# Optimization experiments

Measured on AMD Instinct MI355X. Metric: run time of the kernel, lower is better.

The kernel has to match this reference:

```python
import jax, jax.numpy as jnp
import numpy as np

N = 100000   # nodes
E = 500000   # edges
DN = 64      # node feat dim
DE = 64      # edge feat dim
D = 128      # hidden = in_feats = out_feats
TD = 64      # time-encoding dim


def setup_inputs() -> dict:
    key = jax.random.key(0)
    ks = jax.random.split(key, 20)
    s = 0.05
    inp = {
        'nfeat': jax.random.normal(ks[0], (N, DN), dtype=jnp.float32),
        'efeat': jax.random.normal(ks[1], (E, DE), dtype=jnp.float32),
        'src': jax.random.randint(ks[2], (E,), 0, N),
        'dst': jax.random.randint(ks[3], (E,), 0, N),
        'ts': jax.random.uniform(ks[4], (E,), dtype=jnp.float32) * 1000.0,
    }
    i = 5
    for l in (1, 2):
        inp[f'W_self{l}'] = jax.random.normal(ks[i], (D + TD, D), dtype=jnp.float32) * s; i += 1
        inp[f'b_self{l}'] = jnp.zeros((D,), dtype=jnp.float32)
        inp[f'W_neigh{l}'] = jax.random.normal(ks[i], (D, D), dtype=jnp.float32) * s; i += 1
        inp[f'b_neigh{l}'] = jnp.zeros((D,), dtype=jnp.float32)
        inp[f'omega{l}'] = jax.random.normal(ks[i], (TD,), dtype=jnp.float32); i += 1
        inp[f'phase{l}'] = jax.random.normal(ks[i], (TD,), dtype=jnp.float32); i += 1
    return inp


def _tsage_layer(src_prev, dst_prev, src, dst, ts, W_self, b_self, W_neigh, b_neigh, omega, phase):
    # cosine time encoding per edge: [E, TD]
    te = jnp.cos(ts[:, None] * omega[None, :] + phase[None, :])
    # temporal-neighborhood mean: per node, mean of features of incident edges
    sum_n = (jax.ops.segment_sum(dst_prev, src, num_segments=N)
             + jax.ops.segment_sum(src_prev, dst, num_segments=N))      # [N, D]
    ones = jnp.ones((src.shape[0], 1), dtype=src_prev.dtype)
    cnt = (jax.ops.segment_sum(ones, src, num_segments=N)
           + jax.ops.segment_sum(ones, dst, num_segments=N))            # [N, 1]
    mean_n = sum_n / jnp.maximum(cnt, 1.0)                              # [N, D]
    neigh_proj = mean_n @ W_neigh + b_neigh                             # project once per node
    src_out = jnp.concatenate([src_prev, te], axis=1) @ W_self + b_self + neigh_proj[src]
    dst_out = jnp.concatenate([dst_prev, te], axis=1) @ W_self + b_self + neigh_proj[dst]
    # dropout in eval mode (identity), then activation (relu)
    return jax.nn.relu(src_out), jax.nn.relu(dst_out)


def reference(nfeat, efeat, src, dst, ts,
              W_self1, b_self1, W_neigh1, b_neigh1, omega1, phase1,
              W_self2, b_self2, W_neigh2, b_neigh2, omega2, phase2):
    # combine_feats: per-edge gather-concat of endpoint node feats with edge feats
    src_feat = jnp.concatenate([nfeat[src], efeat], axis=1)  # [E, D]
    dst_feat = jnp.concatenate([nfeat[dst], efeat], axis=1)  # [E, D]
    params = [
        (W_self1, b_self1, W_neigh1, b_neigh1, omega1, phase1),
        (W_self2, b_self2, W_neigh2, b_neigh2, omega2, phase2),
    ]
    for p in params:
        src_feat, dst_feat = _tsage_layer(src_feat, dst_feat, src, dst, ts, *p)
    return src_feat, dst_feat
```

## Files before the change

### kernel.cpp

```cpp
#include <hip/hip_runtime.h>
#include <cstdint>
#include <cmath>

#define NN 100000
#define EE 500000
#define CAP 48

typedef __attribute__((ext_vector_type(8))) short short8v;
typedef __attribute__((ext_vector_type(4))) float f32x4;

static __device__ __forceinline__ unsigned short f2bf_rne(float x) {
    unsigned u = __float_as_uint(x);
    u += 0x7FFFu + ((u >> 16) & 1u);
    return (unsigned short)(u >> 16);
}

static __device__ __forceinline__ void split8(float4 a, float4 b,
                                              short8v* hi, short8v* lo) {
    union { short8v v; unsigned u[4]; } H, L;
    float f[8] = {a.x, a.y, a.z, a.w, b.x, b.y, b.z, b.w};
#pragma unroll
    for (int p = 0; p < 4; ++p) {
        unsigned u0 = __float_as_uint(f[2 * p]);
        unsigned u1 = __float_as_uint(f[2 * p + 1]);
        H.u[p] = (u0 >> 16) | (u1 & 0xFFFF0000u);
        float r0 = f[2 * p]     - __uint_as_float(u0 & 0xFFFF0000u);
        float r1 = f[2 * p + 1] - __uint_as_float(u1 & 0xFFFF0000u);
        L.u[p] = (unsigned)f2bf_rne(r0) | ((unsigned)f2bf_rne(r1) << 16);
    }
    *hi = H.v; *lo = L.v;
}

static __device__ __forceinline__ void lds_dma16(const void* g, void* l) {
    __builtin_amdgcn_global_load_lds(
        (const __attribute__((address_space(1))) unsigned int*)g,
        (__attribute__((address_space(3))) unsigned int*)l, 16, 0, 0);
}

__global__ __launch_bounds__(256) void k_build(const int* __restrict__ src,
                                               const int* __restrict__ dst,
                                               int* __restrict__ pos,
                                               int2* __restrict__ inc) {
    int e = blockIdx.x * 256 + threadIdx.x;
    if (e >= EE) return;
    int s = src[e], d = dst[e];
    int sl = atomicAdd(&pos[s], 1);
    if (sl < CAP) inc[(size_t)s * CAP + sl] = make_int2((e << 1) | 1, d);
    int dl = atomicAdd(&pos[d], 1);
    if (dl < CAP) inc[(size_t)d * CAP + dl] = make_int2((e << 1), s);
}

__global__ __launch_bounds__(256) void k_wt2(const float* __restrict__ Wself,
                                             const float* __restrict__ Wneigh,
                                             unsigned short* __restrict__ H,
                                             unsigned short* __restrict__ L) {
    int idx = blockIdx.x * 256 + threadIdx.x;
    if (idx >= 320 * 128) return;
    int k = idx >> 7, c = idx & 127;
    float x = (k < 192) ? Wself[k * 128 + c] : Wneigh[(k - 192) * 128 + c];
    unsigned u = __float_as_uint(x);
    H[(size_t)c * 320 + k] = (unsigned short)(u >> 16);
    float r = x - __uint_as_float(u & 0xFFFF0000u);
    L[(size_t)c * 320 + k] = f2bf_rne(r);
}

template <int LAYER>
__global__ __launch_bounds__(256) void k_agg(const float* __restrict__ featS,
                                             const float* __restrict__ featD,
                                             const float* __restrict__ nfeat,
                                             const float* __restrict__ efeat,
                                             const int* __restrict__ pos,
                                             const int2* __restrict__ inc,
                                             float* __restrict__ mean) {
    int w = (blockIdx.x * 256 + threadIdx.x) >> 6;
    int lane = threadIdx.x & 63;
    if (w >= NN) return;
    int q = lane >> 4, cl = lane & 15;
    int d = pos[w];
    int dd = min(d, CAP);
    const int2* lst = inc + (size_t)w * CAP;
    float a0 = 0.f, a1 = 0.f, a2 = 0.f, a3 = 0.f;
    float a4 = 0.f, a5 = 0.f, a6 = 0.f, a7 = 0.f;
    int2 en = (q < dd) ? lst[q] : make_int2(0, 0);
    for (int j = q; j < dd; j += 4) {
        int2 nxt = (j + 4 < dd) ? lst[j + 4] : en;
        int e = en.x >> 1, side = en.x & 1;
        const float* p;
        if (LAYER == 1) {
            p = (cl < 8) ? (nfeat + (size_t)en.y * 64 + cl * 8)
                         : (efeat + (size_t)e * 64 + (cl - 8) * 8);
        } else {
            p = (side ? featD : featS) + (size_t)e * 128 + cl * 8;
        }
        float4 v0 = *(const float4*)p;
        float4 v1 = *(const float4*)(p + 4);
        a0 += v0.x; a1 += v0.y; a2 += v0.z; a3 += v0.w;
        a4 += v1.x; a5 += v1.y; a6 += v1.z; a7 += v1.w;
        en = nxt;
    }
#pragma unroll
    for (int m = 16; m <= 32; m <<= 1) {
        a0 += __shfl_xor(a0, m); a1 += __shfl_xor(a1, m);
        a2 += __shfl_xor(a2, m); a3 += __shfl_xor(a3, m);
        a4 += __shfl_xor(a4, m); a5 += __shfl_xor(a5, m);
        a6 += __shfl_xor(a6, m); a7 += __shfl_xor(a7, m);
    }
    if (q == 0) {
        float inv = 1.0f / fmaxf((float)d, 1.0f);
        float4 r0, r1;
        r0.x = a0 * inv; r0.y = a1 * inv; r0.z = a2 * inv; r0.w = a3 * inv;
        r1.x = a4 * inv; r1.y = a5 * inv; r1.z = a6 * inv; r1.w = a7 * inv;
        *(float4*)(mean + (size_t)w * 128 + cl * 8) = r0;
        *(float4*)(mean + (size_t)w * 128 + cl * 8 + 4) = r1;
    }
}

template <int LAYER>
__global__ __launch_bounds__(256) void k_edge_fused(
        const float* __restrict__ featS, const float* __restrict__ featD,
        const float* __restrict__ nfeat, const float* __restrict__ efeat,
        const float* __restrict__ mean,
        float* __restrict__ outS, float* __restrict__ outD,
        const int* __restrict__ src, const int* __restrict__ dst,
        const float* __restrict__ ts,
        const unsigned short* __restrict__ WtH,
        const unsigned short* __restrict__ WtL,
        const float* __restrict__ bs, const float* __restrict__ bn,
        const float* __restrict__ omega, const float* __restrict__ phase) {
    __shared__ float Abuf[3][128][32];
    __shared__ unsigned short teH[64][72];
    __shared__ unsigned short teL[64][72];

    const int tid  = threadIdx.x;
    const int e0   = blockIdx.x * 64;
    const int lane = tid & 63;
    const int w    = tid >> 6;
    const int wr   = w >> 1, wc = w & 1;
    const int krow = lane & 15;
    const int kgrp = lane >> 4;

    {
        const int tl = tid & 63;
        const int j0 = (tid >> 6) * 16;
        const float tval = ts[min(e0 + tl, EE - 1)];
#pragma unroll
        for (int j = 0; j < 16; j += 2) {
            int jj = j0 + j;
            float c0 = cosf(fmaf(tval, omega[jj],     phase[jj]));
            float c1 = cosf(fmaf(tval, omega[jj + 1], phase[jj + 1]));
            unsigned u0 = __float_as_uint(c0), u1 = __float_as_uint(c1);
            *(unsigned*)&teH[tl][jj] = (u0 >> 16) | (u1 & 0xFFFF0000u);
            float r0 = c0 - __uint_as_float(u0 & 0xFFFF0000u);
            float r1 = c1 - __uint_as_float(u1 & 0xFFFF0000u);
            *(unsigned*)&teL[tl][jj] =
                (unsigned)f2bf_rne(r0) | ((unsigned)f2bf_rne(r1) << 16);
        }
    }
    asm volatile("s_waitcnt lgkmcnt(0)" ::: "memory");
    __builtin_amdgcn_sched_barrier(0);

    int nodeq[4];
    const float* gbF[4];
    const float* gbE[4];
#pragma unroll
    for (int qq = 0; qq < 4; ++qq) {
        int row = w * 32 + qq * 8 + (lane >> 3);
        int e = min(e0 + (row & 63), EE - 1);
        int node = (row < 64) ? src[e] : dst[e];
        nodeq[qq] = node;
        if (LAYER == 1) {
            gbF[qq] = nfeat + (size_t)node * 64;
            gbE[qq] = efeat + (size_t)e * 64;
        } else {
            gbF[qq] = ((row < 64) ? featS : featD) + (size_t)e * 128;
            gbE[qq] = nullptr;
        }
    }
    const int pslot = lane & 7;

    auto dma = [&](int j) {
#pragma unroll
        for (int qq = 0; qq < 4; ++qq) {
            int row = w * 32 + qq * 8 + (lane >> 3);
            int pg = (pslot - row) & 7;
            const float* gsrc;
            if (j < 4) {
                if (LAYER == 1)
                    gsrc = (j < 2) ? (gbF[qq] + j * 32 + pg * 4)
                                   : (gbE[qq] + (j - 2) * 32 + pg * 4);
                else
                    gsrc = gbF[qq] + j * 32 + pg * 4;
            } else {
                gsrc = mean + (size_t)nodeq[qq] * 128 + (j - 4) * 32 + pg * 4;
            }
            lds_dma16(gsrc, &Abuf[j % 3][(w * 4 + qq) * 8][0]);
        }
    };

    f32x4 acc[4][4] = {};

    dma(0);
    dma(1);
    asm volatile("s_waitcnt vmcnt(4)" ::: "memory");
    __builtin_amdgcn_sched_barrier(0);

#pragma unroll
    for (int j = 0; j < 8; ++j) {
        const int kb = (j < 4) ? j * 32 : 192 + (j - 4) * 32;
        __builtin_amdgcn_s_barrier();
        __builtin_amdgcn_sched_barrier(0);

        const int koff = kb + kgrp * 8;
        short8v Bh[4], Bl[4];
#pragma unroll
        for (int ct = 0; ct < 4; ++ct) {
            int c = wc * 64 + ct * 16 + krow;
            Bh[ct] = *(const short8v*)(WtH + (size_t)c * 320 + koff);
            Bl[ct] = *(const short8v*)(WtL + (size_t)c * 320 + koff);
        }
        __builtin_amdgcn_sched_barrier(0);
        if (j < 6) dma(j + 2);
        __builtin_amdgcn_sched_barrier(0);
        if (j < 7) { asm volatile("s_waitcnt vmcnt(4)" ::: "memory"); }
        else       { asm volatile("s_waitcnt vmcnt(0)" ::: "memory"); }
        __builtin_amdgcn_sched_barrier(0);

        short8v Ah[4], Al[4];
        const int b = j % 3;
#pragma unroll
        for (int rt = 0; rt < 4; ++rt) {
            int row = wr * 64 + rt * 16 + krow;
            float4 x0 = *(const float4*)&Abuf[b][row][(((2 * kgrp)     + row) & 7) * 4];
            float4 x1 = *(const float4*)&Abuf[b][row][(((2 * kgrp + 1) + row) & 7) * 4];
            split8(x0, x1, &Ah[rt], &Al[rt]);
        }
#pragma unroll
        for (int ct = 0; ct < 4; ++ct)
#pragma unroll
            for (int rt = 0; rt < 4; ++rt) {
                acc[rt][ct] = __builtin_amdgcn_mfma_f32_16x16x32_bf16(Ah[rt], Bh[ct], acc[rt][ct], 0, 0, 0);
                acc[rt][ct] = __builtin_amdgcn_mfma_f32_16x16x32_bf16(Ah[rt], Bl[ct], acc[rt][ct], 0, 0, 0);
                acc[rt][ct] = __builtin_amdgcn_mfma_f32_16x16x32_bf16(Al[rt], Bh[ct], acc[rt][ct], 0, 0, 0);
            }
    }

#pragma unroll
    for (int tc = 0; tc < 2; ++tc) {
        const int kb = 128 + tc * 32;
        const int koff = kb + kgrp * 8;
        const int kt = tc * 32 + kgrp * 8;
        short8v Bh[4], Bl[4];
#pragma unroll
        for (int ct = 0; ct < 4; ++ct) {
            int c = wc * 64 + ct * 16 + krow;
            Bh[ct] = *(const short8v*)(WtH + (size_t)c * 320 + koff);
            Bl[ct] = *(const short8v*)(WtL + (size_t)c * 320 + koff);
        }
        short8v Ah[4], Al[4];
#pragma unroll
        for (int rt = 0; rt < 4; ++rt) {
            int el = rt * 16 + krow;
            Ah[rt] = *(const short8v*)&teH[el][kt];
            Al[rt] = *(const short8v*)&teL[el][kt];
        }
#pragma unroll
        for (int ct = 0; ct < 4; ++ct)
#pragma unroll
            for (int rt = 0; rt < 4; ++rt) {
                acc[rt][ct] = __builtin_amdgcn_mfma_f32_16x16x32_bf16(Ah[rt], Bh[ct], acc[rt][ct], 0, 0, 0);
                acc[rt][ct] = __builtin_amdgcn_mfma_f32_16x16x32_bf16(Ah[rt], Bl[ct], acc[rt][ct], 0, 0, 0);
                acc[rt][ct] = __builtin_amdgcn_mfma_f32_16x16x32_bf16(Al[rt], Bh[ct], acc[rt][ct], 0, 0, 0);
            }
    }

    float bcol[4];
#pragma unroll
    for (int ct = 0; ct < 4; ++ct) {
        int col = wc * 64 + ct * 16 + krow;
        bcol[ct] = bs[col] + bn[col];
    }
#pragma unroll
    for (int rt = 0; rt < 4; ++rt)
#pragma unroll
        for (int jj = 0; jj < 4; ++jj) {
            int row = wr * 64 + rt * 16 + kgrp * 4 + jj;
            int e = e0 + (row & 63);
            if (e < EE) {
                float* op = ((row < 64) ? outS : outD) + (size_t)e * 128;
#pragma unroll
                for (int ct = 0; ct < 4; ++ct) {
                    int col = wc * 64 + ct * 16 + krow;
                    op[col] = fmaxf(acc[rt][ct][jj] + bcol[ct], 0.f);
                }
            }
        }
}

extern "C" void kernel_launch(void* const* d_in, const int* in_sizes, int n_in,
                              void* d_out, int out_size, void* d_ws, size_t ws_size,
                              hipStream_t stream) {
    const float* nfeat = (const float*)d_in[0];
    const float* efeat = (const float*)d_in[1];
    const int*   src   = (const int*)d_in[2];
    const int*   dst   = (const int*)d_in[3];
    const float* ts    = (const float*)d_in[4];
    const float* Wself[2]  = {(const float*)d_in[5],  (const float*)d_in[11]};
    const float* bself[2]  = {(const float*)d_in[6],  (const float*)d_in[12]};
    const float* Wneigh[2] = {(const float*)d_in[7],  (const float*)d_in[13]};
    const float* bneigh[2] = {(const float*)d_in[8],  (const float*)d_in[14]};
    const float* omega[2]  = {(const float*)d_in[9],  (const float*)d_in[15]};
    const float* phase[2]  = {(const float*)d_in[10], (const float*)d_in[16]};

    float* outS = (float*)d_out;
    float* outD = outS + (size_t)EE * 128;

    float* mean = (float*)d_ws;
    int*   pos  = (int*)(mean + (size_t)NN * 128);
    int2*  inc  = (int2*)(pos + NN);
    unsigned short* wb = (unsigned short*)(inc + (size_t)NN * CAP);
    unsigned short* WH[2] = {wb,                 wb + 2 * 320 * 128};
    unsigned short* WL[2] = {wb + 320 * 128,     wb + 3 * 320 * 128};

    hipMemsetAsync(pos, 0, NN * sizeof(int), stream);
    k_build<<<(EE + 255) / 256, 256, 0, stream>>>(src, dst, pos, inc);
    for (int l = 0; l < 2; ++l)
        k_wt2<<<(320 * 128 + 255) / 256, 256, 0, stream>>>(Wself[l], Wneigh[l], WH[l], WL[l]);

    k_agg<1><<<(NN * 64 + 255) / 256, 256, 0, stream>>>(outS, outD, nfeat, efeat,
                                                        pos, inc, mean);
    k_edge_fused<1><<<(EE + 63) / 64, 256, 0, stream>>>(outS, outD, nfeat, efeat, mean,
                                                        outS, outD, src, dst, ts,
                                                        WH[0], WL[0], bself[0], bneigh[0],
                                                        omega[0], phase[0]);

    k_agg<2><<<(NN * 64 + 255) / 256, 256, 0, stream>>>(outS, outD, nfeat, efeat,
                                                        pos, inc, mean);
    k_edge_fused<2><<<(EE + 63) / 64, 256, 0, stream>>>(outS, outD, nfeat, efeat, mean,
                                                        outS, outD, src, dst, ts,
                                                        WH[1], WL[1], bself[1], bneigh[1],
                                                        omega[1], phase[1]);
}
```

Before: 1.854 ms.

## Double-buffer edge GEMM staging, interleave weight hi/lo, raise occupancy hint

Shrinks the LDS staging buffer from triple to double buffering, which cuts shared memory so three blocks can fit per CU (launch bounds now request 3). Issues the first DMA before the cosine time-encoding setup so the two overlap. Interleaves the bf16 hi and lo weight halves into one layout so both come from adjacent addresses. It also uses 32-bit byte offsets instead of 64-bit pointers and splits the MFMA work into two halves to lower register pressure. In exchange, prefetch depth drops to one stage and a full vmcnt(0) wait plus barrier now runs every k-step, which may expose load latency.

```diff
diff --git a/kernel.cpp b/kernel.cpp
--- a/kernel.cpp
+++ b/kernel.cpp
@@ -52,16 +52,17 @@
 
 __global__ __launch_bounds__(256) void k_wt2(const float* __restrict__ Wself,
                                              const float* __restrict__ Wneigh,
-                                             unsigned short* __restrict__ H,
-                                             unsigned short* __restrict__ L) {
+                                             unsigned short* __restrict__ WI) {
     int idx = blockIdx.x * 256 + threadIdx.x;
     if (idx >= 320 * 128) return;
     int k = idx >> 7, c = idx & 127;
     float x = (k < 192) ? Wself[k * 128 + c] : Wneigh[(k - 192) * 128 + c];
     unsigned u = __float_as_uint(x);
-    H[(size_t)c * 320 + k] = (unsigned short)(u >> 16);
+    int grp = k >> 3, pos = k & 7;
+    size_t base = (size_t)c * 640 + grp * 16;
+    WI[base + pos] = (unsigned short)(u >> 16);
     float r = x - __uint_as_float(u & 0xFFFF0000u);
-    L[(size_t)c * 320 + k] = f2bf_rne(r);
+    WI[base + 8 + pos] = f2bf_rne(r);
 }
 
 template <int LAYER>
@@ -116,18 +117,17 @@
 }
 
 template <int LAYER>
-__global__ __launch_bounds__(256) void k_edge_fused(
-        const float* __restrict__ featS, const float* __restrict__ featD,
+__global__ __launch_bounds__(256, 3) void k_edge_fused(
+        const float* __restrict__ featS,
         const float* __restrict__ nfeat, const float* __restrict__ efeat,
         const float* __restrict__ mean,
         float* __restrict__ outS, float* __restrict__ outD,
         const int* __restrict__ src, const int* __restrict__ dst,
         const float* __restrict__ ts,
-        const unsigned short* __restrict__ WtH,
-        const unsigned short* __restrict__ WtL,
+        const unsigned short* __restrict__ WI,
         const float* __restrict__ bs, const float* __restrict__ bn,
         const float* __restrict__ omega, const float* __restrict__ phase) {
-    __shared__ float Abuf[3][128][32];
+    __shared__ float Abuf[2][128][32];
     __shared__ unsigned short teH[64][72];
     __shared__ unsigned short teL[64][72];
 
@@ -138,6 +138,44 @@
     const int wr   = w >> 1, wc = w & 1;
     const int krow = lane & 15;
     const int kgrp = lane >> 4;
+    const int pslot = lane & 7;
+
+    unsigned offF[4], offE[4], offM[4];
+#pragma unroll
+    for (int qq = 0; qq < 4; ++qq) {
+        int row = w * 32 + qq * 8 + (lane >> 3);
+        int e = min(e0 + (row & 63), EE - 1);
+        int node = (row < 64) ? src[e] : dst[e];
+        offM[qq] = (unsigned)node * 512u;
+        if (LAYER == 1) {
+            offF[qq] = (unsigned)node * 256u;
+            offE[qq] = (unsigned)e * 256u;
+        } else {
+            offF[qq] = ((row < 64) ? 0u : (unsigned)EE * 512u) + (unsigned)e * 512u;
+            offE[qq] = 0u;
+        }
+    }
+
+    auto dma = [&](int j) {
+#pragma unroll
+        for (int qq = 0; qq < 4; ++qq) {
+            int row = w * 32 + qq * 8 + (lane >> 3);
+            int pg = (pslot - row) & 7;
+            const char* g;
+            if (j < 4) {
+                if (LAYER == 1)
+                    g = (j < 2) ? ((const char*)nfeat + offF[qq] + j * 128 + pg * 16)
+                                : ((const char*)efeat + offE[qq] + (j - 2) * 128 + pg * 16);
+                else
+                    g = (const char*)featS + offF[qq] + j * 128 + pg * 16;
+            } else {
+                g = (const char*)mean + offM[qq] + (j - 4) * 128 + pg * 16;
+            }
+            lds_dma16(g, &Abuf[j & 1][(w * 4 + qq) * 8][0]);
+        }
+    };
+
+    dma(0);
 
     {
         const int tl = tid & 63;
@@ -159,118 +197,89 @@
     asm volatile("s_waitcnt lgkmcnt(0)" ::: "memory");
     __builtin_amdgcn_sched_barrier(0);
 
-    int nodeq[4];
-    const float* gbF[4];
-    const float* gbE[4];
-#pragma unroll
-    for (int qq = 0; qq < 4; ++qq) {
-        int row = w * 32 + qq * 8 + (lane >> 3);
-        int e = min(e0 + (row & 63), EE - 1);
-        int node = (row < 64) ? src[e] : dst[e];
-        nodeq[qq] = node;
-        if (LAYER == 1) {
-            gbF[qq] = nfeat + (size_t)node * 64;
-            gbE[qq] = efeat + (size_t)e * 64;
-        } else {
-            gbF[qq] = ((row < 64) ? featS : featD) + (size_t)e * 128;
-            gbE[qq] = nullptr;
-        }
-    }
-    const int pslot = lane & 7;
-
-    auto dma = [&](int j) {
-#pragma unroll
-        for (int qq = 0; qq < 4; ++qq) {
-            int row = w * 32 + qq * 8 + (lane >> 3);
-            int pg = (pslot - row) & 7;
-            const float* gsrc;
-            if (j < 4) {
-                if (LAYER == 1)
-                    gsrc = (j < 2) ? (gbF[qq] + j * 32 + pg * 4)
-                                   : (gbE[qq] + (j - 2) * 32 + pg * 4);
-                else
-                    gsrc = gbF[qq] + j * 32 + pg * 4;
-            } else {
-                gsrc = mean + (size_t)nodeq[qq] * 128 + (j - 4) * 32 + pg * 4;
-            }
-            lds_dma16(gsrc, &Abuf[j % 3][(w * 4 + qq) * 8][0]);
-        }
-    };
-
     f32x4 acc[4][4] = {};
 
-    dma(0);
-    dma(1);
-    asm volatile("s_waitcnt vmcnt(4)" ::: "memory");
-    __builtin_amdgcn_sched_barrier(0);
-
 #pragma unroll
     for (int j = 0; j < 8; ++j) {
-        const int kb = (j < 4) ? j * 32 : 192 + (j - 4) * 32;
+        asm volatile("s_waitcnt vmcnt(0) lgkmcnt(0)" ::: "memory");
+        __builtin_amdgcn_sched_barrier(0);
         __builtin_amdgcn_s_barrier();
         __builtin_amdgcn_sched_barrier(0);
 
-        const int koff = kb + kgrp * 8;
+        const int kb = (j < 4) ? j * 32 : 192 + (j - 4) * 32;
+        const int goff = ((kb >> 3) + kgrp) * 16;
         short8v Bh[4], Bl[4];
 #pragma unroll
         for (int ct = 0; ct < 4; ++ct) {
             int c = wc * 64 + ct * 16 + krow;
-            Bh[ct] = *(const short8v*)(WtH + (size_t)c * 320 + koff);
-            Bl[ct] = *(const short8v*)(WtL + (size_t)c * 320 + koff);
+            const unsigned short* bp = WI + (size_t)c * 640 + goff;
+            Bh[ct] = *(const short8v*)bp;
+            Bl[ct] = *(const short8v*)(bp + 8);
         }
         __builtin_amdgcn_sched_barrier(0);
-        if (j < 6) dma(j + 2);
+        if (j < 7) dma(j + 1);
         __builtin_amdgcn_sched_barrier(0);
-        if (j < 7) { asm volatile("s_waitcnt vmcnt(4)" ::: "memory"); }
-        else       { asm volatile("s_waitcnt vmcnt(0)" ::: "memory"); }
-        __builtin_amdgcn_sched_barrier(0);
-
-        short8v Ah[4], Al[4];
-        const int b = j % 3;
-#pragma unroll
-        for (int rt = 0; rt < 4; ++rt) {
-            int row = wr * 64 + rt * 16 + krow;
-            float4 x0 = *(const float4*)&Abuf[b][row][(((2 * kgrp)     + row) & 7) * 4];
-            float4 x1 = *(const float4*)&Abuf[b][row][(((2 * kgrp + 1) + row) & 7) * 4];
-            split8(x0, x1, &Ah[rt], &Al[rt]);
-        }
-#pragma unroll
-        for (int ct = 0; ct < 4; ++ct)
-#pragma unroll
-            for (int rt = 0; rt < 4; ++rt) {
-                acc[rt][ct] = __builtin_amdgcn_mfma_f32_16x16x32_bf16(Ah[rt], Bh[ct], acc[rt][ct], 0, 0, 0);
-                acc[rt][ct] = __builtin_amdgcn_mfma_f32_16x16x32_bf16(Ah[rt], Bl[ct], acc[rt][ct], 0, 0, 0);
-                acc[rt][ct] = __builtin_amdgcn_mfma_f32_16x16x32_bf16(Al[rt], Bh[ct], acc[rt][ct], 0, 0, 0);
-            }
+
+        const int b = j & 1;
+#pragma unroll
+        for (int half = 0; half < 2; ++half) {
+            short8v Ah[2], Al[2];
+#pragma unroll
+            for (int r2 = 0; r2 < 2; ++r2) {
+                int row = wr * 64 + (half * 2 + r2) * 16 + krow;
+                float4 x0 = *(const float4*)&Abuf[b][row][(((2 * kgrp)     + row) & 7) * 4];
+                float4 x1 = *(const float4*)&Abuf[b][row][(((2 * kgrp + 1) + row) & 7) * 4];
+                split8(x0, x1, &Ah[r2], &Al[r2]);
+            }
+            if (half == 0) {
+                if (j < 7) { asm volatile("s_waitcnt vmcnt(4)" ::: "memory"); }
+                else       { asm volatile("s_waitcnt vmcnt(0)" ::: "memory"); }
+                __builtin_amdgcn_sched_barrier(0);
+            }
+#pragma unroll
+            for (int ct = 0; ct < 4; ++ct)
+#pragma unroll
+                for (int r2 = 0; r2 < 2; ++r2) {
+                    int rt = half * 2 + r2;
+                    acc[rt][ct] = __builtin_amdgcn_mfma_f32_16x16x32_bf16(Ah[r2], Bh[ct], acc[rt][ct], 0, 0, 0);
+                    acc[rt][ct] = __builtin_amdgcn_mfma_f32_16x16x32_bf16(Ah[r2], Bl[ct], acc[rt][ct], 0, 0, 0);
+                    acc[rt][ct] = __builtin_amdgcn_mfma_f32_16x16x32_bf16(Al[r2], Bh[ct], acc[rt][ct], 0, 0, 0);
+                }
+        }
     }
 
 #pragma unroll
     for (int tc = 0; tc < 2; ++tc) {
         const int kb = 128 + tc * 32;
-        const int koff = kb + kgrp * 8;
+        const int goff = ((kb >> 3) + kgrp) * 16;
         const int kt = tc * 32 + kgrp * 8;
         short8v Bh[4], Bl[4];
 #pragma unroll
         for (int ct = 0; ct < 4; ++ct) {
             int c = wc * 64 + ct * 16 + krow;
-            Bh[ct] = *(const short8v*)(WtH + (size_t)c * 320 + koff);
-            Bl[ct] = *(const short8v*)(WtL + (size_t)c * 320 + koff);
-        }
-        short8v Ah[4], Al[4];
-#pragma unroll
-        for (int rt = 0; rt < 4; ++rt) {
-            int el = rt * 16 + krow;
-            Ah[rt] = *(const short8v*)&teH[el][kt];
-            Al[rt] = *(const short8v*)&teL[el][kt];
-        }
-#pragma unroll
-        for (int ct = 0; ct < 4; ++ct)
-#pragma unroll
-            for (int rt = 0; rt < 4; ++rt) {
-                acc[rt][ct] = __builtin_amdgcn_mfma_f32_16x16x32_bf16(Ah[rt], Bh[ct], acc[rt][ct], 0, 0, 0);
-                acc[rt][ct] = __builtin_amdgcn_mfma_f32_16x16x32_bf16(Ah[rt], Bl[ct], acc[rt][ct], 0, 0, 0);
-                acc[rt][ct] = __builtin_amdgcn_mfma_f32_16x16x32_bf16(Al[rt], Bh[ct], acc[rt][ct], 0, 0, 0);
-            }
+            const unsigned short* bp = WI + (size_t)c * 640 + goff;
+            Bh[ct] = *(const short8v*)bp;
+            Bl[ct] = *(const short8v*)(bp + 8);
+        }
+#pragma unroll
+        for (int half = 0; half < 2; ++half) {
+            short8v Ah[2], Al[2];
+#pragma unroll
+            for (int r2 = 0; r2 < 2; ++r2) {
+                int el = (half * 2 + r2) * 16 + krow;
+                Ah[r2] = *(const short8v*)&teH[el][kt];
+                Al[r2] = *(const short8v*)&teL[el][kt];
+            }
+#pragma unroll
+            for (int ct = 0; ct < 4; ++ct)
+#pragma unroll
+                for (int r2 = 0; r2 < 2; ++r2) {
+                    int rt = half * 2 + r2;
+                    acc[rt][ct] = __builtin_amdgcn_mfma_f32_16x16x32_bf16(Ah[r2], Bh[ct], acc[rt][ct], 0, 0, 0);
+                    acc[rt][ct] = __builtin_amdgcn_mfma_f32_16x16x32_bf16(Ah[r2], Bl[ct], acc[rt][ct], 0, 0, 0);
+                    acc[rt][ct] = __builtin_amdgcn_mfma_f32_16x16x32_bf16(Al[r2], Bh[ct], acc[rt][ct], 0, 0, 0);
+                }
+        }
     }
 
     float bcol[4];
@@ -317,26 +326,25 @@
     float* mean = (float*)d_ws;
     int*   pos  = (int*)(mean + (size_t)NN * 128);
     int2*  inc  = (int2*)(pos + NN);
-    unsigned short* wb = (unsigned short*)(inc + (size_t)NN * CAP);
-    unsigned short* WH[2] = {wb,                 wb + 2 * 320 * 128};
-    unsigned short* WL[2] = {wb + 320 * 128,     wb + 3 * 320 * 128};
+    unsigned short* wi = (unsigned short*)(inc + (size_t)NN * CAP);
+    unsigned short* WIl[2] = {wi, wi + (size_t)128 * 640};
 
     hipMemsetAsync(pos, 0, NN * sizeof(int), stream);
     k_build<<<(EE + 255) / 256, 256, 0, stream>>>(src, dst, pos, inc);
     for (int l = 0; l < 2; ++l)
-        k_wt2<<<(320 * 128 + 255) / 256, 256, 0, stream>>>(Wself[l], Wneigh[l], WH[l], WL[l]);
+        k_wt2<<<(320 * 128 + 255) / 256, 256, 0, stream>>>(Wself[l], Wneigh[l], WIl[l]);
 
     k_agg<1><<<(NN * 64 + 255) / 256, 256, 0, stream>>>(outS, outD, nfeat, efeat,
                                                         pos, inc, mean);
-    k_edge_fused<1><<<(EE + 63) / 64, 256, 0, stream>>>(outS, outD, nfeat, efeat, mean,
+    k_edge_fused<1><<<(EE + 63) / 64, 256, 0, stream>>>(outS, nfeat, efeat, mean,
                                                         outS, outD, src, dst, ts,
-                                                        WH[0], WL[0], bself[0], bneigh[0],
+                                                        WIl[0], bself[0], bneigh[0],
                                                         omega[0], phase[0]);
 
     k_agg<2><<<(NN * 64 + 255) / 256, 256, 0, stream>>>(outS, outD, nfeat, efeat,
                                                         pos, inc, mean);
-    k_edge_fused<2><<<(EE + 63) / 64, 256, 0, stream>>>(outS, outD, nfeat, efeat, mean,
+    k_edge_fused<2><<<(EE + 63) / 64, 256, 0, stream>>>(outS, nfeat, efeat, mean,
                                                         outS, outD, src, dst, ts,
-                                                        WH[1], WL[1], bself[1], bneigh[1],
+                                                        WIl[1], bself[1], bneigh[1],
                                                         omega[1], phase[1]);
 }
```

New measurement: 1.711 ms. -7.7%, faster.
